# Kernel optimization log

Hardware: AMD Instinct MI355X
Metric: run time of the kernel (lower is better)

The kernel has to match this reference:

```python
import jax, jax.numpy as jnp
import numpy as np

V, T, D, L, H, F = 32000, 1024, 768, 8, 12, 3072
DH = D // H
SCALE = 1.0 / np.sqrt(DH)
EPS = 1e-5


def layer_norm(x, w, b):
    mu = jnp.mean(x, axis=-1, keepdims=True)
    var = jnp.mean(jnp.square(x - mu), axis=-1, keepdims=True)
    return (x - mu) * jax.lax.rsqrt(var + EPS) * w + b


def setup_inputs() -> dict:
    key = jax.random.key(0)
    ks = jax.random.split(key, 10)
    def nrm(k, shape, std=0.02):
        return (jax.random.normal(k, shape, dtype=jnp.float32) * std)
    inp = {
        "idx": jax.random.randint(ks[0], (4, T), 0, V, dtype=jnp.int32),
        "targets": jax.random.randint(ks[1], (4, T), 0, V, dtype=jnp.int32),
        "tok_emb": nrm(ks[2], (V, D)),
        "pos_emb": nrm(ks[3], (T, D)),
        "qkv_w": nrm(ks[4], (L, 3 * D, D)),
        "qkv_b": jnp.zeros((L, 3 * D), jnp.float32),
        "proj_w": nrm(ks[5], (L, D, D)),
        "proj_b": jnp.zeros((L, D), jnp.float32),
        "fc1_w": nrm(ks[6], (L, F, D)),
        "fc1_b": jnp.zeros((L, F), jnp.float32),
        "fc2_w": nrm(ks[7], (L, D, F)),
        "fc2_b": jnp.zeros((L, D), jnp.float32),
        "ln1_w": jnp.ones((L, D), jnp.float32),
        "ln1_b": jnp.zeros((L, D), jnp.float32),
        "ln2_w": jnp.ones((L, D), jnp.float32),
        "ln2_b": jnp.zeros((L, D), jnp.float32),
        "lnf_w": jnp.ones((D,), jnp.float32),
        "lnf_b": jnp.zeros((D,), jnp.float32),
    }
    return inp


def gpt_forward(idx, targets, tok_emb, pos_emb, qkv_w, qkv_b, proj_w, proj_b,
                fc1_w, fc1_b, fc2_w, fc2_b, ln1_w, ln1_b, ln2_w, ln2_b, lnf_w, lnf_b):
    B, Tc = idx.shape
    x = tok_emb[idx] + pos_emb[:Tc][None]  # [B,T,D]
    causal = jnp.tril(jnp.ones((Tc, Tc), bool))

    def block(x, p):
        qw, qb, pw, pb, f1w, f1b, f2w, f2b, l1w, l1b, l2w, l2b = p
        h = layer_norm(x, l1w, l1b)
        qkv = h @ qw.T + qb  # [B,T,3D]
        q, k, v = jnp.split(qkv, 3, axis=-1)
        q = q.reshape(B, Tc, H, DH).transpose(0, 2, 1, 3)  # [B,H,T,DH]
        k = k.reshape(B, Tc, H, DH).transpose(0, 2, 1, 3)
        v = v.reshape(B, Tc, H, DH).transpose(0, 2, 1, 3)
        att = jnp.einsum('bhqd,bhkd->bhqk', q, k) * SCALE
        att = jnp.where(causal, att, -jnp.inf)
        att = jax.nn.softmax(att, axis=-1)
        y = jnp.einsum('bhqk,bhkd->bhqd', att, v)
        y = y.transpose(0, 2, 1, 3).reshape(B, Tc, D)
        x = x + y @ pw.T + pb
        h2 = layer_norm(x, l2w, l2b)
        x = x + jax.nn.gelu(h2 @ f1w.T + f1b, approximate=False) @ f2w.T + f2b
        return x, None

    x, _ = jax.lax.scan(block, x, (qkv_w, qkv_b, proj_w, proj_b,
                                   fc1_w, fc1_b, fc2_w, fc2_b,
                                   ln1_w, ln1_b, ln2_w, ln2_b))
    x = layer_norm(x, lnf_w, lnf_b)
    logits = jnp.einsum('btd,vd->btv', x, tok_emb)  # tied lm_head, output_mult=1
    logp = jax.nn.log_softmax(logits, axis=-1)
    valid = targets != -100
    tgt = jnp.where(valid, targets, 0)
    nll = -jnp.take_along_axis(logp, tgt[..., None], axis=-1)[..., 0]
    loss = jnp.sum(nll * valid) / jnp.maximum(jnp.sum(valid), 1)
    return logits, loss


def reference(idx, targets, tok_emb, pos_emb, qkv_w, qkv_b, proj_w, proj_b,
              fc1_w, fc1_b, fc2_w, fc2_b, ln1_w, ln1_b, ln2_w, ln2_b, lnf_w, lnf_b):
    return gpt_forward(idx, targets, tok_emb, pos_emb, qkv_w, qkv_b, proj_w, proj_b,
                       fc1_w, fc1_b, fc2_w, fc2_b, ln1_w, ln1_b, ln2_w, ln2_b, lnf_w, lnf_b)
```

## Files before the change

### kernel.cpp

```cpp
#include <hip/hip_runtime.h>
#include <hip/hip_bf16.h>
#include <math.h>

#define BATCH 4
#define T 1024
#define D 768
#define L 8
#define H 12
#define F 3072
#define V 32000
#define DH 64
#define M (BATCH*T)
#define D3 (3*D)
#define SCALE 0.125f
#define VCHUNK 6400
#define PBT 125

typedef unsigned short u16;
typedef __attribute__((ext_vector_type(8))) short bf16x8;
typedef __attribute__((ext_vector_type(4))) float f32x4;

__device__ inline u16 f2b(float f) {
  __hip_bfloat16 h = __float2bfloat16(f);
  return *(u16*)&h;
}

__device__ inline void gll16(const void* g, void* l) {
  __builtin_amdgcn_global_load_lds(
      (const __attribute__((address_space(1))) unsigned int*)g,
      (__attribute__((address_space(3))) unsigned int*)l, 16, 0, 0);
}

__device__ inline int swzi(int r, int c) {
  return (r * 64 + c) ^ ((((r & 7) ^ ((r >> 3) & 7))) << 3);
}

__device__ inline float block_reduce(float v, bool is_max, float* buf4) {
  int lane = threadIdx.x & 63, wid = threadIdx.x >> 6;
#pragma unroll
  for (int off = 32; off; off >>= 1) {
    float o = __shfl_down(v, off, 64);
    v = is_max ? fmaxf(v, o) : v + o;
  }
  if (lane == 0) buf4[wid] = v;
  __syncthreads();
  float r = is_max ? fmaxf(fmaxf(buf4[0], buf4[1]), fmaxf(buf4[2], buf4[3]))
                   : buf4[0] + buf4[1] + buf4[2] + buf4[3];
  __syncthreads();
  return r;
}

__global__ __launch_bounds__(256) void k_embed(const int* __restrict__ idx,
                                               const float* __restrict__ tok,
                                               const float* __restrict__ pos,
                                               float* __restrict__ x) {
  int i = blockIdx.x * 256 + threadIdx.x;
  int row = i / D, d = i - row * D;
  int t = row & (T - 1);
  x[i] = tok[(size_t)idx[row] * D + d] + pos[(size_t)t * D + d];
}

__global__ __launch_bounds__(256) void k_cvt(const float* __restrict__ in,
                                             u16* __restrict__ out, int n4) {
  int i = blockIdx.x * 256 + threadIdx.x;
  if (i >= n4) return;
  float4 v = ((const float4*)in)[i];
  ushort4 o;
  o.x = f2b(v.x); o.y = f2b(v.y); o.z = f2b(v.z); o.w = f2b(v.w);
  ((ushort4*)out)[i] = o;
}

__global__ __launch_bounds__(256) void k_lnorm(const float* __restrict__ x,
                                               const float* __restrict__ w,
                                               const float* __restrict__ b,
                                               u16* __restrict__ out) {
  int lane = threadIdx.x & 63, wid = threadIdx.x >> 6;
  int row = blockIdx.x * 4 + wid;
  const float4* xr = (const float4*)(x + (size_t)row * D);
  float4 v[3];
  float s = 0.f, ss = 0.f;
#pragma unroll
  for (int p = 0; p < 3; ++p) {
    v[p] = xr[lane + 64 * p];
    s += v[p].x + v[p].y + v[p].z + v[p].w;
    ss += v[p].x * v[p].x + v[p].y * v[p].y + v[p].z * v[p].z + v[p].w * v[p].w;
  }
#pragma unroll
  for (int off = 32; off; off >>= 1) {
    s += __shfl_xor(s, off, 64);
    ss += __shfl_xor(ss, off, 64);
  }
  float mu = s * (1.0f / D);
  float var = ss * (1.0f / D) - mu * mu;
  float rs = rsqrtf(var + 1e-5f);
  ushort4* orow = (ushort4*)(out + (size_t)row * D);
#pragma unroll
  for (int p = 0; p < 3; ++p) {
    float4 wv = ((const float4*)w)[lane + 64 * p];
    float4 bv = ((const float4*)b)[lane + 64 * p];
    ushort4 o;
    o.x = f2b((v[p].x - mu) * rs * wv.x + bv.x);
    o.y = f2b((v[p].y - mu) * rs * wv.y + bv.y);
    o.z = f2b((v[p].z - mu) * rs * wv.z + bv.z);
    o.w = f2b((v[p].w - mu) * rs * wv.w + bv.w);
    orow[lane + 64 * p] = o;
  }
}

__global__ __launch_bounds__(512, 2) void k_gemm8(
    const u16* __restrict__ A, const u16* __restrict__ W,
    const float* __restrict__ bias, const float* __restrict__ resid,
    void* __restrict__ Cout, int K, int ldC, int flags) {
  __shared__ __attribute__((aligned(16))) u16 lds[2][2][128 * 64];
  int tid = threadIdx.x, w = tid >> 6, lane = tid & 63;
  int wm = w >> 2, wn = w & 3;
  int bn = blockIdx.x, bm = blockIdx.y;
  int frow = lane & 15, g = lane >> 4;
  int sr = lane >> 3, scu = lane & 7;
  const u16* Ab = A + (size_t)bm * 128 * K;
  const u16* Wb = W + (size_t)bn * 128 * K;
  int NT = K >> 6;

  f32x4 acc[4][2];
#pragma unroll
  for (int i = 0; i < 4; ++i)
#pragma unroll
    for (int j = 0; j < 2; ++j) acc[i][j] = (f32x4)(0.f);

#define STG(t)                                                            \
  {                                                                       \
    _Pragma("unroll") for (int rr = 0; rr < 2; ++rr) {                    \
      int row = rr * 64 + w * 8 + sr;                                     \
      int gcu = scu ^ (row & 7);                                          \
      gll16(Ab + (size_t)row * K + (t) * 64 + gcu * 8,                    \
            &lds[(t) & 1][0][(rr * 64 + w * 8) * 64]);                    \
      gll16(Wb + (size_t)row * K + (t) * 64 + gcu * 8,                    \
            &lds[(t) & 1][1][(rr * 64 + w * 8) * 64]);                    \
    }                                                                     \
  }

  STG(0);
  asm volatile("s_waitcnt vmcnt(0)");
  __builtin_amdgcn_s_barrier();

  for (int t = 0; t < NT; ++t) {
    if (t + 1 < NT) {
      STG(t + 1);
      asm volatile("s_waitcnt vmcnt(4)");
    } else {
      asm volatile("s_waitcnt vmcnt(0)");
    }
    __builtin_amdgcn_s_barrier();
    const u16* bA = &lds[t & 1][0][0];
    const u16* bB = &lds[t & 1][1][0];
    bf16x8 ar[8], br[4];
#pragma unroll
    for (int i = 0; i < 4; ++i)
#pragma unroll
      for (int kk = 0; kk < 2; ++kk) {
        int r = wm * 64 + i * 16 + frow;
        ar[i * 2 + kk] = *(const bf16x8*)(bA + r * 64 + ((g + kk * 4) ^ (r & 7)) * 8);
      }
#pragma unroll
    for (int j = 0; j < 2; ++j)
#pragma unroll
      for (int kk = 0; kk < 2; ++kk) {
        int r = wn * 32 + j * 16 + frow;
        br[j * 2 + kk] = *(const bf16x8*)(bB + r * 64 + ((g + kk * 4) ^ (r & 7)) * 8);
      }
    __builtin_amdgcn_s_setprio(1);
#pragma unroll
    for (int i = 0; i < 4; ++i)
#pragma unroll
      for (int j = 0; j < 2; ++j)
#pragma unroll
        for (int kk = 0; kk < 2; ++kk)
          acc[i][j] = __builtin_amdgcn_mfma_f32_16x16x32_bf16(
              ar[i * 2 + kk], br[j * 2 + kk], acc[i][j], 0, 0, 0);
    __builtin_amdgcn_s_setprio(0);
    __builtin_amdgcn_s_barrier();
  }
#undef STG

  int m0 = bm * 128 + wm * 64 + g * 4;
  int n0 = bn * 128 + wn * 32 + frow;
#pragma unroll
  for (int i = 0; i < 4; ++i) {
#pragma unroll
    for (int j = 0; j < 2; ++j) {
      int n = n0 + j * 16;
      float bv = (flags & 1) ? bias[n] : 0.f;
#pragma unroll
      for (int q = 0; q < 4; ++q) {
        int m = m0 + i * 16 + q;
        size_t off = (size_t)m * ldC + n;
        float v = acc[i][j][q] + bv;
        if (flags & 4) v = 0.5f * v * (1.0f + erff(v * 0.70710678118f));
        if (flags & 2) v += resid[off];
        if (flags & 8) ((u16*)Cout)[off] = f2b(v);
        else           ((float*)Cout)[off] = v;
      }
    }
  }
}

__global__ __launch_bounds__(512, 2) void k_lm256(
    const u16* __restrict__ A,
    const u16* __restrict__ B,
    float* __restrict__ C,
    float* __restrict__ pm, float* __restrict__ ps,
    int gc0) {
  __shared__ __attribute__((aligned(16))) u16 lds[2][2][2][128 * 64];
  __shared__ float pml[256][4], psl[256][4];
  const int K = 768, NT = 12;
  int tid = threadIdx.x, w = tid >> 6, lane = tid & 63;
  int wm = w >> 2, wn = w & 3;
  int bm = blockIdx.y, bn = blockIdx.x;
  int frow = lane & 15, g = lane >> 4;
  int sr = lane >> 3, scu = lane & 7;
  const u16* Abase = A + (size_t)bm * 256 * K;
  const u16* Bbase = B + (size_t)bn * 256 * K;

  f32x4 acc[8][4];
#pragma unroll
  for (int i = 0; i < 8; ++i)
#pragma unroll
    for (int j = 0; j < 4; ++j) acc[i][j] = (f32x4)(0.f);

#define STAGE(t, h)                                                       \
  {                                                                       \
    const u16* src = ((h) < 2 ? Abase : Bbase) + (size_t)(((h)&1) * 128) * K; \
    u16* dst = &lds[(t) & 1][(h) >> 1][(h)&1][0];                         \
    _Pragma("unroll") for (int rr = 0; rr < 2; ++rr) {                    \
      int row = rr * 64 + w * 8 + sr;                                     \
      int gcu = scu ^ (row & 7);                                          \
      gll16(src + (size_t)row * K + (t) * 64 + gcu * 8,                   \
            dst + (rr * 64 + w * 8) * 64);                                \
    }                                                                     \
  }

  bf16x8 ar[8], br[8];
#define LDA(T_, ILO)                                                      \
  {                                                                       \
    const u16* base = &lds[(T_)&1][0][wm][0];                             \
    _Pragma("unroll") for (int ii = 0; ii < 4; ++ii)                      \
    _Pragma("unroll") for (int kk = 0; kk < 2; ++kk) {                    \
      int ri = ((ILO) + ii) * 16 + frow;                                  \
      int u = (g + kk * 4) ^ (ri & 7);                                    \
      ar[ii * 2 + kk] = *(const bf16x8*)(base + ri * 64 + u * 8);         \
    }                                                                     \
  }
#define LDB(T_, JLO, BO)                                                  \
  {                                                                       \
    const u16* base = &lds[(T_)&1][1][wn >> 1][0];                        \
    _Pragma("unroll") for (int jj = 0; jj < 2; ++jj)                      \
    _Pragma("unroll") for (int kk = 0; kk < 2; ++kk) {                    \
      int rj = (wn & 1) * 64 + ((JLO) + jj) * 16 + frow;                  \
      int u = (g + kk * 4) ^ (rj & 7);                                    \
      br[(BO) + jj * 2 + kk] = *(const bf16x8*)(base + rj * 64 + u * 8);  \
    }                                                                     \
  }
#define MFMA16(ILO, JLO, BO)                                              \
  _Pragma("unroll") for (int ii = 0; ii < 4; ++ii)                        \
  _Pragma("unroll") for (int jj = 0; jj < 2; ++jj)                        \
  _Pragma("unroll") for (int kk = 0; kk < 2; ++kk)                        \
    acc[(ILO) + ii][(JLO) + jj] = __builtin_amdgcn_mfma_f32_16x16x32_bf16( \
        ar[ii * 2 + kk], br[(BO) + jj * 2 + kk], acc[(ILO) + ii][(JLO) + jj], 0, 0, 0);

  STAGE(0, 0); STAGE(0, 1); STAGE(0, 2); STAGE(0, 3);
  asm volatile("s_waitcnt vmcnt(0)");
  __builtin_amdgcn_s_barrier();

  for (int t = 0; t < NT; ++t) {
    bool pf = (t + 1 < NT);
    LDA(t, 0); LDB(t, 0, 0);
    if (pf) STAGE(t + 1, 0);
    __builtin_amdgcn_s_setprio(1);
    MFMA16(0, 0, 0);
    __builtin_amdgcn_s_setprio(0);
    __builtin_amdgcn_s_barrier();
    LDB(t, 2, 4);
    if (pf) STAGE(t + 1, 1);
    __builtin_amdgcn_s_setprio(1);
    MFMA16(0, 2, 4);
    __builtin_amdgcn_s_setprio(0);
    __builtin_amdgcn_s_barrier();
    LDA(t, 4);
    if (pf) STAGE(t + 1, 2);
    __builtin_amdgcn_s_setprio(1);
    MFMA16(4, 2, 4);
    __builtin_amdgcn_s_setprio(0);
    __builtin_amdgcn_s_barrier();
    if (pf) STAGE(t + 1, 3);
    __builtin_amdgcn_s_setprio(1);
    MFMA16(4, 0, 0);
    __builtin_amdgcn_s_setprio(0);
    asm volatile("s_waitcnt vmcnt(0)");
    __builtin_amdgcn_s_barrier();
  }

#pragma unroll
  for (int ii = 0; ii < 8; ++ii) {
#pragma unroll
    for (int q = 0; q < 4; ++q) {
      float mx = fmaxf(fmaxf(acc[ii][0][q], acc[ii][1][q]),
                       fmaxf(acc[ii][2][q], acc[ii][3][q]));
      mx = fmaxf(mx, __shfl_xor(mx, 1, 64));
      mx = fmaxf(mx, __shfl_xor(mx, 2, 64));
      mx = fmaxf(mx, __shfl_xor(mx, 4, 64));
      mx = fmaxf(mx, __shfl_xor(mx, 8, 64));
      float sm = 0.f;
#pragma unroll
      for (int jj = 0; jj < 4; ++jj) sm += __expf(acc[ii][jj][q] - mx);
      sm += __shfl_xor(sm, 1, 64);
      sm += __shfl_xor(sm, 2, 64);
      sm += __shfl_xor(sm, 4, 64);
      sm += __shfl_xor(sm, 8, 64);
      int lrow = wm * 128 + ii * 16 + g * 4 + q;
      if (frow == 0) { pml[lrow][wn] = mx; psl[lrow][wn] = sm; }
      size_t off = (size_t)(bm * 256 + lrow) * V + gc0 + bn * 256 + wn * 64 + frow;
#pragma unroll
      for (int jj = 0; jj < 4; ++jj) C[off + jj * 16] = acc[ii][jj][q];
    }
  }
  __syncthreads();
  if (tid < 256) {
    float m = fmaxf(fmaxf(pml[tid][0], pml[tid][1]), fmaxf(pml[tid][2], pml[tid][3]));
    float s = 0.f;
#pragma unroll
    for (int w4 = 0; w4 < 4; ++w4) s += psl[tid][w4] * __expf(pml[tid][w4] - m);
    size_t grow = bm * 256 + tid;
    int pb = gc0 / 256 + bn;
    pm[grow * PBT + pb] = m;
    ps[grow * PBT + pb] = s;
  }
#undef STAGE
#undef LDA
#undef LDB
#undef MFMA16
}

__global__ __launch_bounds__(256) void k_fattn(const u16* __restrict__ qkv,
                                               u16* __restrict__ y) {
  __shared__ __attribute__((aligned(16))) u16 lQ[128 * 64];
  __shared__ __attribute__((aligned(16))) u16 lK[64 * 64];
  __shared__ __attribute__((aligned(16))) u16 lVt[64 * 64];
  __shared__ __attribute__((aligned(16))) u16 lP[128 * 64];
  int tid = threadIdx.x;
  int w = tid >> 6, lane = tid & 63;
  int qtb = blockIdx.x;
  int bh = blockIdx.y, b = bh / H, h = bh - b * H;
  int q0 = qtb * 128;
  const u16* base = qkv + (size_t)b * T * D3 + h * DH;
  int srow = lane >> 3;
  int scu = lane & 7;
  int frow = lane & 15, g = lane >> 4;
  int w16 = w * 16;
  int qrow = g * 4;

#pragma unroll
  for (int c = 0; c < 4; ++c) {
    int row = c * 32 + w * 8 + srow;
    int gcu = scu ^ (row & 7);
    gll16(base + (size_t)(q0 + row) * D3 + gcu * 8, lQ + (c * 32 + w * 8) * 64);
  }

  float m_r[2][4], l_r[2][4];
  f32x4 o[2][4];
#pragma unroll
  for (int s = 0; s < 2; ++s)
#pragma unroll
    for (int i = 0; i < 4; ++i) {
      m_r[s][i] = -1e30f; l_r[s][i] = 0.f; o[s][i] = (f32x4)(0.f);
    }

  int ktmax = 2 * qtb + 1;
  for (int kt = 0; kt <= ktmax; ++kt) {
    __syncthreads();
    int k0 = kt * 64;
#pragma unroll
    for (int c = 0; c < 2; ++c) {
      int row = c * 32 + w * 8 + srow;
      int gcu = scu ^ (row & 7);
      gll16(base + D + (size_t)(k0 + row) * D3 + gcu * 8, lK + (c * 32 + w * 8) * 64);
    }
#pragma unroll
    for (int p = 0; p < 2; ++p) {
      int kk = p * 32 + w * 8 + srow;
      uint4 vv = *(const uint4*)(base + 2 * D + (size_t)(k0 + kk) * D3 + scu * 8);
      unsigned vals[4] = {vv.x, vv.y, vv.z, vv.w};
#pragma unroll
      for (int e = 0; e < 4; ++e) {
        lVt[swzi(scu * 8 + 2 * e, kk)]     = (u16)(vals[e] & 0xffff);
        lVt[swzi(scu * 8 + 2 * e + 1, kk)] = (u16)(vals[e] >> 16);
      }
    }
    __syncthreads();

#pragma unroll
    for (int s = 0; s < 2; ++s) {
      if (kt > 2 * qtb + s) continue;
      int qs = s * 64 + w16;
      int f7 = frow & 7;
      bf16x8 aq0 = *(const bf16x8*)(lQ + (qs + frow) * 64 + (g ^ f7) * 8);
      bf16x8 aq1 = *(const bf16x8*)(lQ + (qs + frow) * 64 + ((g + 4) ^ f7) * 8);
      f32x4 sv[4];
#pragma unroll
      for (int kn = 0; kn < 4; ++kn) {
        bf16x8 bk0 = *(const bf16x8*)(lK + (kn * 16 + frow) * 64 + (g ^ f7) * 8);
        bf16x8 bk1 = *(const bf16x8*)(lK + (kn * 16 + frow) * 64 + ((g + 4) ^ f7) * 8);
        sv[kn] = __builtin_amdgcn_mfma_f32_16x16x32_bf16(aq0, bk0, (f32x4)(0.f), 0, 0, 0);
        sv[kn] = __builtin_amdgcn_mfma_f32_16x16x32_bf16(aq1, bk1, sv[kn], 0, 0, 0);
      }
#pragma unroll
      for (int kn = 0; kn < 4; ++kn)
#pragma unroll
        for (int qi = 0; qi < 4; ++qi) {
          float v = sv[kn][qi] * SCALE;
          if (kt == 2 * qtb + s) {
            int qg = q0 + qs + qrow + qi;
            int kg = k0 + kn * 16 + frow;
            if (kg > qg) v = -1e30f;
          }
          sv[kn][qi] = v;
        }
#pragma unroll
      for (int qi = 0; qi < 4; ++qi) {
        float rm = fmaxf(fmaxf(sv[0][qi], sv[1][qi]), fmaxf(sv[2][qi], sv[3][qi]));
        rm = fmaxf(rm, __shfl_xor(rm, 1, 64));
        rm = fmaxf(rm, __shfl_xor(rm, 2, 64));
        rm = fmaxf(rm, __shfl_xor(rm, 4, 64));
        rm = fmaxf(rm, __shfl_xor(rm, 8, 64));
        float mn = fmaxf(m_r[s][qi], rm);
        float alpha = __expf(m_r[s][qi] - mn);
        m_r[s][qi] = mn;
        float rs = 0.f;
#pragma unroll
        for (int kn = 0; kn < 4; ++kn) {
          float p = __expf(sv[kn][qi] - mn);
          sv[kn][qi] = p;
          rs += p;
        }
        rs += __shfl_xor(rs, 1, 64);
        rs += __shfl_xor(rs, 2, 64);
        rs += __shfl_xor(rs, 4, 64);
        rs += __shfl_xor(rs, 8, 64);
        l_r[s][qi] = l_r[s][qi] * alpha + rs;
#pragma unroll
        for (int df = 0; df < 4; ++df) o[s][df][qi] *= alpha;
      }
#pragma unroll
      for (int kn = 0; kn < 4; ++kn)
#pragma unroll
        for (int qi = 0; qi < 4; ++qi)
          lP[swzi(qs + qrow + qi, kn * 16 + frow)] = f2b(sv[kn][qi]);
      bf16x8 pa0 = *(const bf16x8*)(lP + swzi(qs + frow, g * 8));
      bf16x8 pa1 = *(const bf16x8*)(lP + swzi(qs + frow, 32 + g * 8));
#pragma unroll
      for (int df = 0; df < 4; ++df) {
        bf16x8 bv0 = *(const bf16x8*)(lVt + swzi(df * 16 + frow, g * 8));
        bf16x8 bv1 = *(const bf16x8*)(lVt + swzi(df * 16 + frow, 32 + g * 8));
        o[s][df] = __builtin_amdgcn_mfma_f32_16x16x32_bf16(pa0, bv0, o[s][df], 0, 0, 0);
        o[s][df] = __builtin_amdgcn_mfma_f32_16x16x32_bf16(pa1, bv1, o[s][df], 0, 0, 0);
      }
    }
  }

#pragma unroll
  for (int s = 0; s < 2; ++s)
#pragma unroll
    for (int df = 0; df < 4; ++df)
#pragma unroll
      for (int qi = 0; qi < 4; ++qi) {
        int qg = q0 + s * 64 + w16 + qrow + qi;
        y[(size_t)(b * T + qg) * D + h * DH + df * 16 + frow] =
            f2b(o[s][df][qi] / l_r[s][qi]);
      }
}

__global__ __launch_bounds__(256) void k_loss_rows(
    const float* __restrict__ pm, const float* __restrict__ ps,
    const float* __restrict__ logits, const int* __restrict__ targets,
    float* __restrict__ nll) {
  int lane = threadIdx.x & 63, wid = threadIdx.x >> 6;
  int row = blockIdx.x * 4 + wid;
  const float* pmr = pm + (size_t)row * PBT;
  const float* psr = ps + (size_t)row * PBT;
  float m = -1e30f;
  for (int i = lane; i < PBT; i += 64) m = fmaxf(m, pmr[i]);
#pragma unroll
  for (int off = 32; off; off >>= 1) m = fmaxf(m, __shfl_xor(m, off, 64));
  float s = 0.f;
  for (int i = lane; i < PBT; i += 64) s += psr[i] * __expf(pmr[i] - m);
#pragma unroll
  for (int off = 32; off; off >>= 1) s += __shfl_xor(s, off, 64);
  if (lane == 0) {
    int tgt = targets[row];
    nll[row] = (tgt != -100) ? (m + logf(s) - logits[(size_t)row * V + tgt]) : 0.f;
  }
}

__global__ __launch_bounds__(256) void k_loss_final(const float* __restrict__ nll,
                                                    const int* __restrict__ targets,
                                                    float* __restrict__ out) {
  __shared__ float buf4[4];
  float s = 0.f, c = 0.f;
  for (int i = threadIdx.x; i < M; i += 256) {
    s += nll[i];
    c += (targets[i] != -100) ? 1.f : 0.f;
  }
  s = block_reduce(s, false, buf4);
  c = block_reduce(c, false, buf4);
  if (threadIdx.x == 0) out[0] = s / fmaxf(c, 1.f);
}

extern "C" void kernel_launch(void* const* d_in, const int* in_sizes, int n_in,
                              void* d_out, int out_size, void* d_ws, size_t ws_size,
                              hipStream_t stream) {
  const int* idx       = (const int*)d_in[0];
  const int* targets   = (const int*)d_in[1];
  const float* tok     = (const float*)d_in[2];
  const float* pos     = (const float*)d_in[3];
  const float* qkv_w   = (const float*)d_in[4];
  const float* qkv_b   = (const float*)d_in[5];
  const float* proj_w  = (const float*)d_in[6];
  const float* proj_b  = (const float*)d_in[7];
  const float* fc1_w   = (const float*)d_in[8];
  const float* fc1_b   = (const float*)d_in[9];
  const float* fc2_w   = (const float*)d_in[10];
  const float* fc2_b   = (const float*)d_in[11];
  const float* ln1_w   = (const float*)d_in[12];
  const float* ln1_b   = (const float*)d_in[13];
  const float* ln2_w   = (const float*)d_in[14];
  const float* ln2_b   = (const float*)d_in[15];
  const float* lnf_w   = (const float*)d_in[16];
  const float* lnf_b   = (const float*)d_in[17];

  float* logits = (float*)d_out;

  char* ws = (char*)d_ws;
  float* x   = (float*)ws;
  u16* hb    = (u16*)(ws + 12582912);
  u16* yb    = (u16*)(ws + 18874368);
  u16* wb    = (u16*)(ws + 25165824);
  float* pm  = (float*)(ws + 34996224);
  float* ps  = (float*)(ws + 37044224);
  float* nll = (float*)(ws + 39092224);

  u16* qkvb   = (u16*)logits;
  u16* f1b    = (u16*)(logits + 9437184);
  u16* wqkv   = (u16*)(logits + 15728640);
  u16* wproj  = (u16*)(logits + 22806528);
  u16* wfc1   = (u16*)(logits + 25165824);
  u16* wfc2   = (u16*)(logits + 34603008);

  k_cvt<<<(L * D3 * D / 4 + 255) / 256, 256, 0, stream>>>(qkv_w, wqkv, L * D3 * D / 4);
  k_cvt<<<(L * D * D / 4 + 255) / 256, 256, 0, stream>>>(proj_w, wproj, L * D * D / 4);
  k_cvt<<<(L * F * D / 4 + 255) / 256, 256, 0, stream>>>(fc1_w, wfc1, L * F * D / 4);
  k_cvt<<<(L * D * F / 4 + 255) / 256, 256, 0, stream>>>(fc2_w, wfc2, L * D * F / 4);

  k_embed<<<(M * D) / 256, 256, 0, stream>>>(idx, tok, pos, x);

  for (int l = 0; l < L; ++l) {
    k_lnorm<<<M / 4, 256, 0, stream>>>(x, ln1_w + (size_t)l * D, ln1_b + (size_t)l * D, hb);
    k_gemm8<<<dim3(D3 / 128, M / 128), 512, 0, stream>>>(
        hb, wqkv + (size_t)l * D3 * D, qkv_b + (size_t)l * D3, nullptr, qkvb, D, D3, 9);
    k_fattn<<<dim3(T / 128, BATCH * H), 256, 0, stream>>>(qkvb, yb);
    k_gemm8<<<dim3(D / 128, M / 128), 512, 0, stream>>>(
        yb, wproj + (size_t)l * D * D, proj_b + (size_t)l * D, x, x, D, D, 3);
    k_lnorm<<<M / 4, 256, 0, stream>>>(x, ln2_w + (size_t)l * D, ln2_b + (size_t)l * D, hb);
    k_gemm8<<<dim3(F / 128, M / 128), 512, 0, stream>>>(
        hb, wfc1 + (size_t)l * F * D, fc1_b + (size_t)l * F, nullptr, f1b, D, F, 13);
    k_gemm8<<<dim3(D / 128, M / 128), 512, 0, stream>>>(
        f1b, wfc2 + (size_t)l * D * F, fc2_b + (size_t)l * D, x, x, F, D, 3);
  }

  k_lnorm<<<M / 4, 256, 0, stream>>>(x, lnf_w, lnf_b, hb);
  for (int c = 0; c < 5; ++c) {
    k_cvt<<<(VCHUNK * D / 4 + 255) / 256, 256, 0, stream>>>(
        tok + (size_t)c * VCHUNK * D, wb, VCHUNK * D / 4);
    k_lm256<<<dim3(VCHUNK / 256, M / 256), 512, 0, stream>>>(
        hb, wb, logits, pm, ps, c * VCHUNK);
  }
  k_loss_rows<<<M / 4, 256, 0, stream>>>(pm, ps, logits, targets, nll);
  k_loss_final<<<1, 256, 0, stream>>>(nll, targets, logits + (size_t)M * V);
}
```

Measured before the change: 2.169 ms.

## Fuse weight conversions, front-load GEMM staging, register-prefetch K/V in attention

Result: no change. 2.182 ms (+0.6%).

```diff
diff --git a/kernel.cpp b/kernel.cpp
--- a/kernel.cpp
+++ b/kernel.cpp
@@ -65,6 +65,27 @@
   int i = blockIdx.x * 256 + threadIdx.x;
   if (i >= n4) return;
   float4 v = ((const float4*)in)[i];
+  ushort4 o;
+  o.x = f2b(v.x); o.y = f2b(v.y); o.z = f2b(v.z); o.w = f2b(v.w);
+  ((ushort4*)out)[i] = o;
+}
+
+__global__ __launch_bounds__(256) void k_cvtw(const float* __restrict__ q,
+                                              const float* __restrict__ p,
+                                              const float* __restrict__ f1,
+                                              const float* __restrict__ f2,
+                                              u16* __restrict__ out) {
+  const int N0 = L * D3 * D / 4, N1 = L * D * D / 4;
+  const int N2 = L * F * D / 4, N3 = L * D * F / 4;
+  int i = blockIdx.x * 256 + threadIdx.x;
+  if (i >= N0 + N1 + N2 + N3) return;
+  const float* src;
+  int j = i;
+  if (i < N0) { src = q; }
+  else if (i < N0 + N1) { src = p; j = i - N0; }
+  else if (i < N0 + N1 + N2) { src = f1; j = i - N0 - N1; }
+  else { src = f2; j = i - N0 - N1 - N2; }
+  float4 v = ((const float4*)src)[j];
   ushort4 o;
   o.x = f2b(v.x); o.y = f2b(v.y); o.z = f2b(v.z); o.w = f2b(v.w);
   ((ushort4*)out)[i] = o;
@@ -274,24 +295,22 @@
   for (int t = 0; t < NT; ++t) {
     bool pf = (t + 1 < NT);
     LDA(t, 0); LDB(t, 0, 0);
-    if (pf) STAGE(t + 1, 0);
+    if (pf) { STAGE(t + 1, 0); STAGE(t + 1, 1); }
     __builtin_amdgcn_s_setprio(1);
     MFMA16(0, 0, 0);
     __builtin_amdgcn_s_setprio(0);
     __builtin_amdgcn_s_barrier();
     LDB(t, 2, 4);
-    if (pf) STAGE(t + 1, 1);
+    if (pf) { STAGE(t + 1, 2); STAGE(t + 1, 3); }
     __builtin_amdgcn_s_setprio(1);
     MFMA16(0, 2, 4);
     __builtin_amdgcn_s_setprio(0);
     __builtin_amdgcn_s_barrier();
     LDA(t, 4);
-    if (pf) STAGE(t + 1, 2);
     __builtin_amdgcn_s_setprio(1);
     MFMA16(4, 2, 4);
     __builtin_amdgcn_s_setprio(0);
     __builtin_amdgcn_s_barrier();
-    if (pf) STAGE(t + 1, 3);
     __builtin_amdgcn_s_setprio(1);
     MFMA16(4, 0, 0);
     __builtin_amdgcn_s_setprio(0);
@@ -375,27 +394,38 @@
     }
 
   int ktmax = 2 * qtb + 1;
+  uint4 kr[2], vr[2];
+#pragma unroll
+  for (int c = 0; c < 2; ++c) {
+    int row = c * 32 + w * 8 + srow;
+    kr[c] = *(const uint4*)(base + D + (size_t)row * D3 + scu * 8);
+    vr[c] = *(const uint4*)(base + 2 * D + (size_t)row * D3 + scu * 8);
+  }
+
   for (int kt = 0; kt <= ktmax; ++kt) {
     __syncthreads();
     int k0 = kt * 64;
 #pragma unroll
     for (int c = 0; c < 2; ++c) {
       int row = c * 32 + w * 8 + srow;
-      int gcu = scu ^ (row & 7);
-      gll16(base + D + (size_t)(k0 + row) * D3 + gcu * 8, lK + (c * 32 + w * 8) * 64);
-    }
-#pragma unroll
-    for (int p = 0; p < 2; ++p) {
-      int kk = p * 32 + w * 8 + srow;
-      uint4 vv = *(const uint4*)(base + 2 * D + (size_t)(k0 + kk) * D3 + scu * 8);
-      unsigned vals[4] = {vv.x, vv.y, vv.z, vv.w};
+      *(uint4*)(lK + row * 64 + (scu ^ (row & 7)) * 8) = kr[c];
+      unsigned vals[4] = {vr[c].x, vr[c].y, vr[c].z, vr[c].w};
 #pragma unroll
       for (int e = 0; e < 4; ++e) {
-        lVt[swzi(scu * 8 + 2 * e, kk)]     = (u16)(vals[e] & 0xffff);
-        lVt[swzi(scu * 8 + 2 * e + 1, kk)] = (u16)(vals[e] >> 16);
+        lVt[swzi(scu * 8 + 2 * e, row)]     = (u16)(vals[e] & 0xffff);
+        lVt[swzi(scu * 8 + 2 * e + 1, row)] = (u16)(vals[e] >> 16);
       }
     }
     __syncthreads();
+    if (kt < ktmax) {
+      int k0n = k0 + 64;
+#pragma unroll
+      for (int c = 0; c < 2; ++c) {
+        int row = c * 32 + w * 8 + srow;
+        kr[c] = *(const uint4*)(base + D + (size_t)(k0n + row) * D3 + scu * 8);
+        vr[c] = *(const uint4*)(base + 2 * D + (size_t)(k0n + row) * D3 + scu * 8);
+      }
+    }
 
 #pragma unroll
     for (int s = 0; s < 2; ++s) {
@@ -554,10 +584,10 @@
   u16* wfc1   = (u16*)(logits + 25165824);
   u16* wfc2   = (u16*)(logits + 34603008);
 
-  k_cvt<<<(L * D3 * D / 4 + 255) / 256, 256, 0, stream>>>(qkv_w, wqkv, L * D3 * D / 4);
-  k_cvt<<<(L * D * D / 4 + 255) / 256, 256, 0, stream>>>(proj_w, wproj, L * D * D / 4);
-  k_cvt<<<(L * F * D / 4 + 255) / 256, 256, 0, stream>>>(fc1_w, wfc1, L * F * D / 4);
-  k_cvt<<<(L * D * F / 4 + 255) / 256, 256, 0, stream>>>(fc2_w, wfc2, L * D * F / 4);
+  {
+    const int NW4 = (L * D3 * D + L * D * D + L * F * D + L * D * F) / 4;
+    k_cvtw<<<(NW4 + 255) / 256, 256, 0, stream>>>(qkv_w, proj_w, fc1_w, fc2_w, wqkv);
+  }
 
   k_embed<<<(M * D) / 256, 256, 0, stream>>>(idx, tok, pos, x);
 
```
